# Kernel tuning notes

Measured on AMD Instinct MI355X. Metric: run time of the kernel, lower is better.

The kernel has to match this reference:

```python
import jax, jax.numpy as jnp
import numpy as np

B, H, S, D = 4, 16, 2048, 64
NEG = -1000000000.0


def setup_inputs() -> dict:
    key = jax.random.key(0)
    kq, kk, kv, km = jax.random.split(key, 4)
    Q = jax.random.normal(kq, (B, H, S, D), dtype=jnp.float32)
    K = jax.random.normal(kk, (B, H, S, D), dtype=jnp.float32)
    V = jax.random.normal(kv, (B, H, S, D), dtype=jnp.float32)
    attn_mask = jax.random.randint(km, (B, 1, 1, S), 0, 2).astype(jnp.bool_)
    return {"Q": Q, "K": K, "V": V, "attn_mask": attn_mask}


def reference(Q, K, V, attn_mask):
    scale = 1.0 / (Q.shape[-1] ** 0.5)
    # [B,H,S,S] scores, masked, softmax over keys
    scores = jnp.einsum("bhqd,bhkd->bhqk", Q, K) * scale
    scores = jnp.where(attn_mask, NEG, scores)
    attn_prob = jax.nn.softmax(scores, axis=-1)
    context = jnp.einsum("bhqk,bhkd->bhqd", attn_prob, V)
    return context
```

## Files before the change

kernel.cpp:

```cpp
#include <hip/hip_runtime.h>
#include <hip/hip_bf16.h>

#define B_ 4
#define H_ 16
#define S_ 2048
#define D_ 64
#define BH_ (B_ * H_)
#define VSTR 2048

#define QS 0.18033688011112042f

typedef __bf16 bf16_t;
typedef __attribute__((ext_vector_type(8))) bf16_t bf16x8;
typedef __attribute__((ext_vector_type(4))) bf16_t bf16x4;
typedef __attribute__((ext_vector_type(4))) float f32x4;

#if __has_builtin(__builtin_amdgcn_exp2f)
#define EX2(x) __builtin_amdgcn_exp2f(x)
#else
#define EX2(x) exp2f(x)
#endif

#define KC_OFF 0u
#define VT_OFF 16777216u
#define CIDX_OFF 33554432u
#define NK_OFF 33619968u

__device__ __forceinline__ bf16x4 cvt4(const float4 a) {
  return (bf16x4){(bf16_t)a.x, (bf16_t)a.y, (bf16_t)a.z, (bf16_t)a.w};
}

__device__ __forceinline__ void gl2lds16(const bf16_t* g, bf16_t* l) {
  __builtin_amdgcn_global_load_lds(
      (const __attribute__((address_space(1))) unsigned int*)g,
      (__attribute__((address_space(3))) unsigned int*)l, 16, 0, 0);
}

__global__ __launch_bounds__(256) void scan_kernel(const unsigned char* __restrict__ raw,
                                                   int* __restrict__ cidx,
                                                   int* __restrict__ nkarr) {
  const int b = blockIdx.x;
  const int tid = threadIdx.x;
  __shared__ int isBool;
  if (tid == 0) isBool = 0;
  __syncthreads();
  int any = 0;
  for (int i = tid; i < B_ * S_; i += 256)
    if ((i & 3) && raw[i]) any = 1;
  if (any) isBool = 1;
  __syncthreads();
  const bool ib = (isBool != 0);

  int flags[8], cnt = 0;
  const int base = tid * 8;
#pragma unroll
  for (int j = 0; j < 8; ++j) {
    const int key = base + j;
    const int m = ib ? (raw[b * S_ + key] ? 1 : 0)
                     : (((const int*)raw)[b * S_ + key] ? 1 : 0);
    flags[j] = m ? 0 : 1;
    cnt += flags[j];
  }
  __shared__ int sc[256];
  sc[tid] = cnt;
  __syncthreads();
  for (int off = 1; off < 256; off <<= 1) {
    const int v = sc[tid];
    const int u = (tid >= off) ? sc[tid - off] : 0;
    __syncthreads();
    sc[tid] = v + u;
    __syncthreads();
  }
  int pos = (tid > 0) ? sc[tid - 1] : 0;
  const int total = sc[255];
  int* cb = cidx + b * VSTR;
#pragma unroll
  for (int j = 0; j < 8; ++j)
    if (flags[j]) cb[pos++] = base + j;
  if (tid == 0) nkarr[b] = total;
  const int padend = ((total + 63) >> 6) << 6;
  for (int i = total + tid; i < padend; i += 256) cb[i] = 0;
}

__global__ __launch_bounds__(256) void gather_kernel(const float* __restrict__ K,
                                                     const float* __restrict__ V,
                                                     const int* __restrict__ cidx,
                                                     const int* __restrict__ nkarr,
                                                     bf16_t* __restrict__ Kc,
                                                     bf16_t* __restrict__ Vtc) {
  const int blk = blockIdx.x;
  const int bh = blk >> 5, tile = blk & 31;
  const int b = bh >> 4;
  if (tile * 64 >= nkarr[b]) return;
  const int tid = threadIdx.x;
  __shared__ int idx[64];
  __shared__ float T[64][65];
  if (tid < 64) idx[tid] = cidx[b * VSTR + tile * 64 + tid];
  __syncthreads();
  {
    const int row = tid >> 2, g = tid & 3;
    const float* src = K + (size_t)bh * S_ * D_ + (size_t)idx[row] * D_;
    bf16_t* dst = Kc + (size_t)bh * VSTR * D_ + (size_t)(tile * 64 + row) * D_;
#pragma unroll
    for (int c = 0; c < 2; ++c) {
      const float4 lo = *(const float4*)(src + c * 32 + g * 4);
      const float4 hi = *(const float4*)(src + c * 32 + 16 + g * 4);
      *(bf16x4*)(dst + (c * 4 + g) * 8) = cvt4(lo);
      *(bf16x4*)(dst + (c * 4 + g) * 8 + 4) = cvt4(hi);
    }
  }
  const float* vsrc = V + (size_t)bh * S_ * D_;
#pragma unroll
  for (int rep = 0; rep < 4; ++rep) {
    const int i2 = rep * 256 + tid;
    const int row = i2 >> 4, d4 = (i2 & 15) << 2;
    const float4 v = *(const float4*)(vsrc + (size_t)idx[row] * D_ + d4);
    T[row][d4] = v.x; T[row][d4 + 1] = v.y; T[row][d4 + 2] = v.z; T[row][d4 + 3] = v.w;
  }
  __syncthreads();
  bf16_t* vdst = Vtc + (size_t)bh * D_ * VSTR + tile * 64;
#pragma unroll
  for (int rep = 0; rep < 4; ++rep) {
    const int i2 = rep * 256 + tid;
    const int d = i2 >> 4, k4 = (i2 & 15) << 2;
    const int kc = k4 >> 5, within = k4 & 31;
    const int g = (within & 15) >> 2, half = (within & 16) ? 4 : 0;
    const int pos = (kc * 4 + g) * 8 + half;
    const bf16x4 o = {(bf16_t)T[k4][d], (bf16_t)T[k4 + 1][d], (bf16_t)T[k4 + 2][d],
                      (bf16_t)T[k4 + 3][d]};
    *(bf16x4*)(vdst + (size_t)d * VSTR + pos) = o;
  }
}


__device__ __forceinline__ bf16x8 qpack(const float4 a, const float4 b) {
  bf16x8 r;
  r[0] = (bf16_t)(a.x * QS); r[1] = (bf16_t)(a.y * QS);
  r[2] = (bf16_t)(a.z * QS); r[3] = (bf16_t)(a.w * QS);
  r[4] = (bf16_t)(b.x * QS); r[5] = (bf16_t)(b.y * QS);
  r[6] = (bf16_t)(b.z * QS); r[7] = (bf16_t)(b.w * QS);
  return r;
}

__global__ __launch_bounds__(512, 2) void attn_main_kernel(const float* __restrict__ Q,
                                                           const bf16_t* __restrict__ Kc,
                                                           const bf16_t* __restrict__ Vtc,
                                                           const int* __restrict__ nkarr,
                                                           float* __restrict__ out) {
  __shared__ bf16_t Kl[2][64][64];
  __shared__ bf16_t Vl[2][64][64];

  const int bid = blockIdx.x;
  const int wu = (bid & 7) * 64 + (bid >> 3);
  const int qt = wu & 7, bh = wu >> 3, b = bh >> 4;

  const int nk = nkarr[b];
  const int nt = (nk + 63) >> 6;

  const int tid = threadIdx.x, wid = tid >> 6, lane = tid & 63;
  const int gg = (lane >> 4) & 3, g4 = gg << 2, qi = lane & 15;
  const int q7 = qi & 7;
  const int koff0 = ((gg) ^ q7) << 3;
  const int koff1 = ((4 + gg) ^ q7) << 3;

  const size_t bhoff = (size_t)bh * (S_ * D_);
  const bf16_t* Kg = Kc + (size_t)bh * VSTR * D_;
  const bf16_t* Vg = Vtc + (size_t)bh * D_ * VSTR;

  const int qrow0 = qt * 256 + wid * 32 + qi;
  bf16x8 qb[2][2];
#pragma unroll
  for (int g = 0; g < 2; ++g) {
    const float* qp = Q + bhoff + (size_t)(qrow0 + g * 16) * D_;
#pragma unroll
    for (int c = 0; c < 2; ++c)
      qb[g][c] = qpack(*(const float4*)(qp + c * 32 + g4),
                       *(const float4*)(qp + c * 32 + 16 + g4));
  }

  bf16x8 ones;
#pragma unroll
  for (int j = 0; j < 8; ++j) ones[j] = (bf16_t)1.0f;

  const int srow = tid >> 3;
  const int swc = (tid & 7) ^ ((tid >> 3) & 7);
  const bf16_t* Kgsw = Kg + (size_t)srow * D_ + swc * 8;
  const bf16_t* Vgsw = Vg + (size_t)srow * VSTR + swc * 8;
  bf16_t* KldsBase0 = &Kl[0][wid * 8][0];
  bf16_t* KldsBase1 = &Kl[1][wid * 8][0];
  bf16_t* VldsBase0 = &Vl[0][wid * 8][0];
  bf16_t* VldsBase1 = &Vl[1][wid * 8][0];

  gl2lds16(Kgsw, KldsBase0);
  gl2lds16(Vgsw, VldsBase0);
  __syncthreads();

  f32x4 o[2][4];
#pragma unroll
  for (int g = 0; g < 2; ++g)
#pragma unroll
    for (int dt = 0; dt < 4; ++dt) o[g][dt] = (f32x4){0.f, 0.f, 0.f, 0.f};
  f32x4 la0 = {0.f, 0.f, 0.f, 0.f}, la1 = la0;

  for (int t = 0; t < nt; ++t) {
    const int cur = t & 1;
    const bool more = (t + 1 < nt);
    const int kv = (t + 1) * 64;
    const int rem = nk - t * 64;

    if (more) {
      gl2lds16(Kgsw + (size_t)kv * D_, cur ? KldsBase0 : KldsBase1);
      gl2lds16(Vgsw + kv, cur ? VldsBase0 : VldsBase1);
    }

    bf16x8 pb0[2], pb1[2];
    __builtin_amdgcn_s_setprio(1);
#pragma unroll
    for (int kt = 0; kt < 4; ++kt) {
      const bf16_t* krow = &Kl[cur][kt * 16 + qi][0];
      f32x4 a0 = {0.f, 0.f, 0.f, 0.f}, a1 = a0;
      {
        const bf16x8 ka = *(const bf16x8*)(krow + koff0);
        a0 = __builtin_amdgcn_mfma_f32_16x16x32_bf16(ka, qb[0][0], a0, 0, 0, 0);
        a1 = __builtin_amdgcn_mfma_f32_16x16x32_bf16(ka, qb[1][0], a1, 0, 0, 0);
      }
      {
        const bf16x8 ka = *(const bf16x8*)(krow + koff1);
        a0 = __builtin_amdgcn_mfma_f32_16x16x32_bf16(ka, qb[0][1], a0, 0, 0, 0);
        a1 = __builtin_amdgcn_mfma_f32_16x16x32_bf16(ka, qb[1][1], a1, 0, 0, 0);
      }
      if (more) {
#pragma unroll
        for (int r = 0; r < 4; ++r) {
          pb0[kt >> 1][(kt & 1) * 4 + r] = (bf16_t)EX2(a0[r]);
          pb1[kt >> 1][(kt & 1) * 4 + r] = (bf16_t)EX2(a1[r]);
        }
      } else {
#pragma unroll
        for (int r = 0; r < 4; ++r) {
          const int kidx = kt * 16 + g4 + r;
          float p0 = EX2(a0[r]);
          float p1 = EX2(a1[r]);
          p0 = (kidx < rem) ? p0 : 0.f;
          p1 = (kidx < rem) ? p1 : 0.f;
          pb0[kt >> 1][(kt & 1) * 4 + r] = (bf16_t)p0;
          pb1[kt >> 1][(kt & 1) * 4 + r] = (bf16_t)p1;
        }
      }
    }
    __builtin_amdgcn_s_setprio(0);

    __builtin_amdgcn_s_setprio(1);
    la0 = __builtin_amdgcn_mfma_f32_16x16x32_bf16(ones, pb0[0], la0, 0, 0, 0);
    la0 = __builtin_amdgcn_mfma_f32_16x16x32_bf16(ones, pb0[1], la0, 0, 0, 0);
    la1 = __builtin_amdgcn_mfma_f32_16x16x32_bf16(ones, pb1[0], la1, 0, 0, 0);
    la1 = __builtin_amdgcn_mfma_f32_16x16x32_bf16(ones, pb1[1], la1, 0, 0, 0);
#pragma unroll
    for (int dt = 0; dt < 4; ++dt) {
      const bf16_t* vrow = &Vl[cur][dt * 16 + qi][0];
      {
        const bf16x8 va = *(const bf16x8*)(vrow + koff0);
        o[0][dt] = __builtin_amdgcn_mfma_f32_16x16x32_bf16(va, pb0[0], o[0][dt], 0, 0, 0);
        o[1][dt] = __builtin_amdgcn_mfma_f32_16x16x32_bf16(va, pb1[0], o[1][dt], 0, 0, 0);
      }
      {
        const bf16x8 va = *(const bf16x8*)(vrow + koff1);
        o[0][dt] = __builtin_amdgcn_mfma_f32_16x16x32_bf16(va, pb0[1], o[0][dt], 0, 0, 0);
        o[1][dt] = __builtin_amdgcn_mfma_f32_16x16x32_bf16(va, pb1[1], o[1][dt], 0, 0, 0);
      }
    }
    __builtin_amdgcn_s_setprio(0);

    if (more) __syncthreads();
  }

#pragma unroll
  for (int g = 0; g < 2; ++g) {
    const float inv = 1.0f / (g ? la1[0] : la0[0]);
    float* op = out + bhoff + (size_t)(qrow0 + g * 16) * D_;
#pragma unroll
    for (int dt = 0; dt < 4; ++dt) {
      float4 w;
      w.x = o[g][dt][0] * inv;
      w.y = o[g][dt][1] * inv;
      w.z = o[g][dt][2] * inv;
      w.w = o[g][dt][3] * inv;
      *(float4*)(op + dt * 16 + g4) = w;
    }
  }
}

extern "C" void kernel_launch(void* const* d_in, const int* in_sizes, int n_in,
                              void* d_out, int out_size, void* d_ws, size_t ws_size,
                              hipStream_t stream) {
  const float* Q = (const float*)d_in[0];
  const float* K = (const float*)d_in[1];
  const float* V = (const float*)d_in[2];
  const unsigned char* mraw = (const unsigned char*)d_in[3];
  float* out = (float*)d_out;

  char* ws = (char*)d_ws;
  bf16_t* Kc = (bf16_t*)(ws + KC_OFF);
  bf16_t* Vtc = (bf16_t*)(ws + VT_OFF);
  int* cidx = (int*)(ws + CIDX_OFF);
  int* nkarr = (int*)(ws + NK_OFF);

  scan_kernel<<<B_, 256, 0, stream>>>(mraw, cidx, nkarr);
  gather_kernel<<<BH_ * 32, 256, 0, stream>>>(K, V, cidx, nkarr, Kc, Vtc);
  attn_main_kernel<<<512, 512, 0, stream>>>(Q, Kc, Vtc, nkarr, out);
}
```

Measured before the change: 70.11 us.

## Split key range across two blocks per query tile and combine partial outputs

Adds a split-K (flash-decoding style) path: each query tile's compacted key range is split in half across two blocks, giving 1024 blocks instead of 512. Each half writes unnormalized partial outputs and row sums to workspace, and a new combine kernel adds them and normalizes. This targets under-occupancy of the GPU's compute units with 512 blocks. In exchange it costs an extra kernel launch plus about 32MB of extra fp32 writes and reads, and it requires enough workspace or falls back to the old path.

```diff
diff --git a/kernel.cpp b/kernel.cpp
--- a/kernel.cpp
+++ b/kernel.cpp
@@ -25,6 +25,9 @@
 #define VT_OFF 16777216u
 #define CIDX_OFF 33554432u
 #define NK_OFF 33619968u
+#define L_OFF 33685504u
+#define O1_OFF 34734080u
+#define WS_NEED2 (O1_OFF + 33554432u)
 
 __device__ __forceinline__ bf16x4 cvt4(const float4 a) {
   return (bf16x4){(bf16_t)a.x, (bf16_t)a.y, (bf16_t)a.z, (bf16_t)a.w};
@@ -142,20 +145,38 @@
   return r;
 }
 
+template <int NSPLIT>
 __global__ __launch_bounds__(512, 2) void attn_main_kernel(const float* __restrict__ Q,
                                                            const bf16_t* __restrict__ Kc,
                                                            const bf16_t* __restrict__ Vtc,
                                                            const int* __restrict__ nkarr,
-                                                           float* __restrict__ out) {
+                                                           float* __restrict__ out,
+                                                           float* __restrict__ lws,
+                                                           float* __restrict__ O1) {
   __shared__ bf16_t Kl[2][64][64];
   __shared__ bf16_t Vl[2][64][64];
 
   const int bid = blockIdx.x;
-  const int wu = (bid & 7) * 64 + (bid >> 3);
-  const int qt = wu & 7, bh = wu >> 3, b = bh >> 4;
+  int split, qt, bh;
+  if (NSPLIT == 2) {
+    const int wu = (bid & 7) * 128 + (bid >> 3);
+    split = wu & 1;
+    const int rest = wu >> 1;
+    qt = rest & 7;
+    bh = rest >> 3;
+  } else {
+    const int wu = (bid & 7) * 64 + (bid >> 3);
+    split = 0;
+    qt = wu & 7;
+    bh = wu >> 3;
+  }
+  const int b = bh >> 4;
 
   const int nk = nkarr[b];
   const int nt = (nk + 63) >> 6;
+  const int h0 = (nt + 1) >> 1;
+  const int tstart = (NSPLIT == 2 && split) ? h0 : 0;
+  const int tend = (NSPLIT == 2 && !split) ? h0 : nt;
 
   const int tid = threadIdx.x, wid = tid >> 6, lane = tid & 63;
   const int gg = (lane >> 4) & 3, g4 = gg << 2, qi = lane & 15;
@@ -191,10 +212,6 @@
   bf16_t* VldsBase0 = &Vl[0][wid * 8][0];
   bf16_t* VldsBase1 = &Vl[1][wid * 8][0];
 
-  gl2lds16(Kgsw, KldsBase0);
-  gl2lds16(Vgsw, VldsBase0);
-  __syncthreads();
-
   f32x4 o[2][4];
 #pragma unroll
   for (int g = 0; g < 2; ++g)
@@ -202,92 +219,137 @@
     for (int dt = 0; dt < 4; ++dt) o[g][dt] = (f32x4){0.f, 0.f, 0.f, 0.f};
   f32x4 la0 = {0.f, 0.f, 0.f, 0.f}, la1 = la0;
 
-  for (int t = 0; t < nt; ++t) {
-    const int cur = t & 1;
-    const bool more = (t + 1 < nt);
-    const int kv = (t + 1) * 64;
-    const int rem = nk - t * 64;
-
-    if (more) {
-      gl2lds16(Kgsw + (size_t)kv * D_, cur ? KldsBase0 : KldsBase1);
-      gl2lds16(Vgsw + kv, cur ? VldsBase0 : VldsBase1);
-    }
-
-    bf16x8 pb0[2], pb1[2];
-    __builtin_amdgcn_s_setprio(1);
-#pragma unroll
-    for (int kt = 0; kt < 4; ++kt) {
-      const bf16_t* krow = &Kl[cur][kt * 16 + qi][0];
-      f32x4 a0 = {0.f, 0.f, 0.f, 0.f}, a1 = a0;
-      {
-        const bf16x8 ka = *(const bf16x8*)(krow + koff0);
-        a0 = __builtin_amdgcn_mfma_f32_16x16x32_bf16(ka, qb[0][0], a0, 0, 0, 0);
-        a1 = __builtin_amdgcn_mfma_f32_16x16x32_bf16(ka, qb[1][0], a1, 0, 0, 0);
-      }
-      {
-        const bf16x8 ka = *(const bf16x8*)(krow + koff1);
-        a0 = __builtin_amdgcn_mfma_f32_16x16x32_bf16(ka, qb[0][1], a0, 0, 0, 0);
-        a1 = __builtin_amdgcn_mfma_f32_16x16x32_bf16(ka, qb[1][1], a1, 0, 0, 0);
-      }
+  if (tstart < tend) {
+    gl2lds16(Kgsw + (size_t)(tstart * 64) * D_, KldsBase0);
+    gl2lds16(Vgsw + tstart * 64, VldsBase0);
+    __syncthreads();
+
+    for (int t = tstart; t < tend; ++t) {
+      const int cur = (t - tstart) & 1;
+      const bool more = (t + 1 < tend);
+      const bool gated = (t == nt - 1);
+      const int rem = nk - t * 64;
+
       if (more) {
-#pragma unroll
-        for (int r = 0; r < 4; ++r) {
-          pb0[kt >> 1][(kt & 1) * 4 + r] = (bf16_t)EX2(a0[r]);
-          pb1[kt >> 1][(kt & 1) * 4 + r] = (bf16_t)EX2(a1[r]);
-        }
-      } else {
-#pragma unroll
-        for (int r = 0; r < 4; ++r) {
-          const int kidx = kt * 16 + g4 + r;
-          float p0 = EX2(a0[r]);
-          float p1 = EX2(a1[r]);
-          p0 = (kidx < rem) ? p0 : 0.f;
-          p1 = (kidx < rem) ? p1 : 0.f;
-          pb0[kt >> 1][(kt & 1) * 4 + r] = (bf16_t)p0;
-          pb1[kt >> 1][(kt & 1) * 4 + r] = (bf16_t)p1;
-        }
-      }
-    }
-    __builtin_amdgcn_s_setprio(0);
-
-    __builtin_amdgcn_s_setprio(1);
-    la0 = __builtin_amdgcn_mfma_f32_16x16x32_bf16(ones, pb0[0], la0, 0, 0, 0);
-    la0 = __builtin_amdgcn_mfma_f32_16x16x32_bf16(ones, pb0[1], la0, 0, 0, 0);
-    la1 = __builtin_amdgcn_mfma_f32_16x16x32_bf16(ones, pb1[0], la1, 0, 0, 0);
-    la1 = __builtin_amdgcn_mfma_f32_16x16x32_bf16(ones, pb1[1], la1, 0, 0, 0);
-#pragma unroll
-    for (int dt = 0; dt < 4; ++dt) {
-      const bf16_t* vrow = &Vl[cur][dt * 16 + qi][0];
-      {
-        const bf16x8 va = *(const bf16x8*)(vrow + koff0);
-        o[0][dt] = __builtin_amdgcn_mfma_f32_16x16x32_bf16(va, pb0[0], o[0][dt], 0, 0, 0);
-        o[1][dt] = __builtin_amdgcn_mfma_f32_16x16x32_bf16(va, pb1[0], o[1][dt], 0, 0, 0);
-      }
-      {
-        const bf16x8 va = *(const bf16x8*)(vrow + koff1);
-        o[0][dt] = __builtin_amdgcn_mfma_f32_16x16x32_bf16(va, pb0[1], o[0][dt], 0, 0, 0);
-        o[1][dt] = __builtin_amdgcn_mfma_f32_16x16x32_bf16(va, pb1[1], o[1][dt], 0, 0, 0);
-      }
-    }
-    __builtin_amdgcn_s_setprio(0);
-
-    if (more) __syncthreads();
-  }
-
-#pragma unroll
-  for (int g = 0; g < 2; ++g) {
-    const float inv = 1.0f / (g ? la1[0] : la0[0]);
-    float* op = out + bhoff + (size_t)(qrow0 + g * 16) * D_;
-#pragma unroll
-    for (int dt = 0; dt < 4; ++dt) {
-      float4 w;
-      w.x = o[g][dt][0] * inv;
-      w.y = o[g][dt][1] * inv;
-      w.z = o[g][dt][2] * inv;
-      w.w = o[g][dt][3] * inv;
-      *(float4*)(op + dt * 16 + g4) = w;
-    }
-  }
+        gl2lds16(Kgsw + (size_t)((t + 1) * 64) * D_, cur ? KldsBase0 : KldsBase1);
+        gl2lds16(Vgsw + (t + 1) * 64, cur ? VldsBase0 : VldsBase1);
+      }
+
+      bf16x8 pb0[2], pb1[2];
+      __builtin_amdgcn_s_setprio(1);
+#pragma unroll
+      for (int kt = 0; kt < 4; ++kt) {
+        const bf16_t* krow = &Kl[cur][kt * 16 + qi][0];
+        f32x4 a0 = {0.f, 0.f, 0.f, 0.f}, a1 = a0;
+        {
+          const bf16x8 ka = *(const bf16x8*)(krow + koff0);
+          a0 = __builtin_amdgcn_mfma_f32_16x16x32_bf16(ka, qb[0][0], a0, 0, 0, 0);
+          a1 = __builtin_amdgcn_mfma_f32_16x16x32_bf16(ka, qb[1][0], a1, 0, 0, 0);
+        }
+        {
+          const bf16x8 ka = *(const bf16x8*)(krow + koff1);
+          a0 = __builtin_amdgcn_mfma_f32_16x16x32_bf16(ka, qb[0][1], a0, 0, 0, 0);
+          a1 = __builtin_amdgcn_mfma_f32_16x16x32_bf16(ka, qb[1][1], a1, 0, 0, 0);
+        }
+        if (!gated) {
+#pragma unroll
+          for (int r = 0; r < 4; ++r) {
+            pb0[kt >> 1][(kt & 1) * 4 + r] = (bf16_t)EX2(a0[r]);
+            pb1[kt >> 1][(kt & 1) * 4 + r] = (bf16_t)EX2(a1[r]);
+          }
+        } else {
+#pragma unroll
+          for (int r = 0; r < 4; ++r) {
+            const int kidx = kt * 16 + g4 + r;
+            float p0 = EX2(a0[r]);
+            float p1 = EX2(a1[r]);
+            p0 = (kidx < rem) ? p0 : 0.f;
+            p1 = (kidx < rem) ? p1 : 0.f;
+            pb0[kt >> 1][(kt & 1) * 4 + r] = (bf16_t)p0;
+            pb1[kt >> 1][(kt & 1) * 4 + r] = (bf16_t)p1;
+          }
+        }
+      }
+      __builtin_amdgcn_s_setprio(0);
+
+      __builtin_amdgcn_s_setprio(1);
+      la0 = __builtin_amdgcn_mfma_f32_16x16x32_bf16(ones, pb0[0], la0, 0, 0, 0);
+      la0 = __builtin_amdgcn_mfma_f32_16x16x32_bf16(ones, pb0[1], la0, 0, 0, 0);
+      la1 = __builtin_amdgcn_mfma_f32_16x16x32_bf16(ones, pb1[0], la1, 0, 0, 0);
+      la1 = __builtin_amdgcn_mfma_f32_16x16x32_bf16(ones, pb1[1], la1, 0, 0, 0);
+#pragma unroll
+      for (int dt = 0; dt < 4; ++dt) {
+        const bf16_t* vrow = &Vl[cur][dt * 16 + qi][0];
+        {
+          const bf16x8 va = *(const bf16x8*)(vrow + koff0);
+          o[0][dt] = __builtin_amdgcn_mfma_f32_16x16x32_bf16(va, pb0[0], o[0][dt], 0, 0, 0);
+          o[1][dt] = __builtin_amdgcn_mfma_f32_16x16x32_bf16(va, pb1[0], o[1][dt], 0, 0, 0);
+        }
+        {
+          const bf16x8 va = *(const bf16x8*)(vrow + koff1);
+          o[0][dt] = __builtin_amdgcn_mfma_f32_16x16x32_bf16(va, pb0[1], o[0][dt], 0, 0, 0);
+          o[1][dt] = __builtin_amdgcn_mfma_f32_16x16x32_bf16(va, pb1[1], o[1][dt], 0, 0, 0);
+        }
+      }
+      __builtin_amdgcn_s_setprio(0);
+
+      if (more) __syncthreads();
+    }
+  }
+
+  if (NSPLIT == 2) {
+    float* tgt = split ? O1 : out;
+#pragma unroll
+    for (int g = 0; g < 2; ++g) {
+      float* op = tgt + bhoff + (size_t)(qrow0 + g * 16) * D_;
+#pragma unroll
+      for (int dt = 0; dt < 4; ++dt) {
+        float4 w;
+        w.x = (g ? o[1] : o[0])[dt][0];
+        w.y = (g ? o[1] : o[0])[dt][1];
+        w.z = (g ? o[1] : o[0])[dt][2];
+        w.w = (g ? o[1] : o[0])[dt][3];
+        *(float4*)(op + dt * 16 + g4) = w;
+      }
+    }
+    if (gg == 0) {
+      float* lp = lws + split * (BH_ * S_) + bh * S_;
+      lp[qrow0] = la0[0];
+      lp[qrow0 + 16] = la1[0];
+    }
+  } else {
+#pragma unroll
+    for (int g = 0; g < 2; ++g) {
+      const float inv = 1.0f / (g ? la1[0] : la0[0]);
+      float* op = out + bhoff + (size_t)(qrow0 + g * 16) * D_;
+#pragma unroll
+      for (int dt = 0; dt < 4; ++dt) {
+        float4 w;
+        w.x = o[g][dt][0] * inv;
+        w.y = o[g][dt][1] * inv;
+        w.z = o[g][dt][2] * inv;
+        w.w = o[g][dt][3] * inv;
+        *(float4*)(op + dt * 16 + g4) = w;
+      }
+    }
+  }
+}
+
+__global__ __launch_bounds__(256) void combine_kernel(float* __restrict__ out,
+                                                      const float* __restrict__ O1,
+                                                      const float* __restrict__ lws) {
+  const int idx = blockIdx.x * 256 + threadIdx.x;
+  const int row = idx >> 4;
+  const float l = lws[row] + lws[BH_ * S_ + row];
+  const float inv = (l > 0.f) ? (1.0f / l) : 0.f;
+  const float4 a = ((const float4*)out)[idx];
+  const float4 c = ((const float4*)O1)[idx];
+  float4 w;
+  w.x = (a.x + c.x) * inv;
+  w.y = (a.y + c.y) * inv;
+  w.z = (a.z + c.z) * inv;
+  w.w = (a.w + c.w) * inv;
+  ((float4*)out)[idx] = w;
 }
 
 extern "C" void kernel_launch(void* const* d_in, const int* in_sizes, int n_in,
@@ -307,5 +369,14 @@
 
   scan_kernel<<<B_, 256, 0, stream>>>(mraw, cidx, nkarr);
   gather_kernel<<<BH_ * 32, 256, 0, stream>>>(K, V, cidx, nkarr, Kc, Vtc);
-  attn_main_kernel<<<512, 512, 0, stream>>>(Q, Kc, Vtc, nkarr, out);
-}
+
+  if (ws_size >= (size_t)WS_NEED2) {
+    float* lws = (float*)(ws + L_OFF);
+    float* O1 = (float*)(ws + O1_OFF);
+    attn_main_kernel<2><<<1024, 512, 0, stream>>>(Q, Kc, Vtc, nkarr, out, lws, O1);
+    const int n4 = BH_ * S_ * D_ / 4;
+    combine_kernel<<<n4 / 256, 256, 0, stream>>>(out, O1, lws);
+  } else {
+    attn_main_kernel<1><<<512, 512, 0, stream>>>(Q, Kc, Vtc, nkarr, out, nullptr, nullptr);
+  }
+}
```

Result: slower. 88.10 us (+25.7%).
